# Kernel tuning notes

Hardware: AMD Instinct MI355X
Metric: run time of the kernel (lower is better)

Reference implementation:

```python
import jax, jax.numpy as jnp
import numpy as np

D_MODEL = 2048
N_HEADS = 32
N_KV_HEADS = 8
HEAD_DIM = D_MODEL // N_HEADS
ROPE_BASE = 10000.0

def setup_inputs() -> dict:
    key = jax.random.key(0)
    ks = jax.random.split(key, 5)
    B, S = 1, 2048
    x = jax.random.normal(ks[0], (B, S, D_MODEL), dtype=jnp.float32)
    sc = 1.0 / np.sqrt(D_MODEL)
    Wq = jax.random.normal(ks[1], (D_MODEL, D_MODEL), dtype=jnp.float32) * sc
    Wk = jax.random.normal(ks[2], (N_KV_HEADS * HEAD_DIM, D_MODEL), dtype=jnp.float32) * sc
    Wv = jax.random.normal(ks[3], (N_KV_HEADS * HEAD_DIM, D_MODEL), dtype=jnp.float32) * sc
    Wo = jax.random.normal(ks[4], (D_MODEL, D_MODEL), dtype=jnp.float32) * sc
    return {"x": x, "Wq": Wq, "Wk": Wk, "Wv": Wv, "Wo": Wo}

def _rope_cos_sin(seq_len, dtype):
    inv_freq = 1.0 / (ROPE_BASE ** (jnp.arange(0, HEAD_DIM, 2, dtype=jnp.float32) / HEAD_DIM))
    t = jnp.arange(seq_len, dtype=jnp.float32)
    freqs = jnp.einsum('i,j->ij', t, inv_freq)          # [S, hd/2]
    emb = jnp.concatenate([freqs, freqs], axis=-1)      # [S, hd]
    return jnp.cos(emb).astype(dtype), jnp.sin(emb).astype(dtype)

def _rotate_half(x):
    x1, x2 = x[..., : HEAD_DIM // 2], x[..., HEAD_DIM // 2 :]
    return jnp.concatenate([-x2, x1], axis=-1)

def reference(x, Wq, Wk, Wv, Wo):
    B, S, _ = x.shape
    scale = HEAD_DIM ** -0.5
    # projections (Linear: x @ W.T)
    q = (x @ Wq.T).reshape(B, S, N_HEADS, HEAD_DIM).transpose(0, 2, 1, 3)      # [B,H,S,hd]
    k = (x @ Wk.T).reshape(B, S, N_KV_HEADS, HEAD_DIM).transpose(0, 2, 1, 3)   # [B,Hkv,S,hd]
    v = (x @ Wv.T).reshape(B, S, N_KV_HEADS, HEAD_DIM).transpose(0, 2, 1, 3)
    cos, sin = _rope_cos_sin(S, x.dtype)                # [S,hd], broadcasts over B,H
    q = q * cos + _rotate_half(q) * sin
    k = k * cos + _rotate_half(k) * sin
    rep = N_HEADS // N_KV_HEADS
    k = jnp.repeat(k, rep, axis=1)                       # [B,H,S,hd]
    v = jnp.repeat(v, rep, axis=1)
    scores = jnp.einsum('bhqd,bhkd->bhqk', q, k) * scale # [B,H,S,S]
    attn = jax.nn.softmax(scores, axis=-1)
    out = jnp.einsum('bhqk,bhkd->bhqd', attn, v)         # [B,H,S,hd]
    out = out.transpose(0, 2, 1, 3).reshape(B, S, D_MODEL)
    return out @ Wo.T
```

## Files before the change

### kernel.cpp

```cpp
#include <hip/hip_runtime.h>
#include <hip/hip_bf16.h>
#include <cmath>

typedef __bf16 bf16_t;
typedef __attribute__((ext_vector_type(8))) __bf16 bf16x8;
typedef __attribute__((ext_vector_type(4))) float f32x4;
typedef __attribute__((ext_vector_type(4))) short s16x4;

#define S_LEN 2048
#define DMODEL 2048
#define KVDIM 512
#define NHEADS 32
#define NKV 8
#define HDIM 64

__device__ inline f32x4 zero4() { f32x4 z; z[0]=0.f; z[1]=0.f; z[2]=0.f; z[3]=0.f; return z; }

__global__ void convert_all(const float* __restrict__ s0, bf16_t* __restrict__ d0,
                            const float* __restrict__ s1, bf16_t* __restrict__ d1,
                            const float* __restrict__ s2, bf16_t* __restrict__ d2,
                            const float* __restrict__ s3, bf16_t* __restrict__ d3,
                            const float* __restrict__ s4, bf16_t* __restrict__ d4) {
  int b = blockIdx.x;
  const float* src; bf16_t* dst; int boff;
  if      (b < 2048) { src = s0; dst = d0; boff = b; }
  else if (b < 4096) { src = s1; dst = d1; boff = b - 2048; }
  else if (b < 4608) { src = s2; dst = d2; boff = b - 4096; }
  else if (b < 5120) { src = s3; dst = d3; boff = b - 4608; }
  else               { src = s4; dst = d4; boff = b - 5120; }
  int idx = (boff * 256 + threadIdx.x) * 8;
  bf16x8 v;
#pragma unroll
  for (int j = 0; j < 8; j++) v[j] = (bf16_t)src[idx + j];
  *(bf16x8*)(dst + idx) = v;
}

template <int BN, bool F32OUT>
__device__ __forceinline__ void gemm_core(const bf16_t* __restrict__ A,
                                          const bf16_t* __restrict__ Bt,
                                          void* __restrict__ Cout,
                                          int N, int K, int bm, int bn) {
  constexpr int NT_W = BN / 32;
  __shared__ __attribute__((aligned(16))) bf16_t As[2][128 * 64];
  __shared__ __attribute__((aligned(16))) bf16_t Bs[2][BN * 64];
  const int tid  = threadIdx.x;
  const int wave = tid >> 6, lane = tid & 63;
  const int wm = wave >> 1, wn = wave & 1;
  const int quad = lane >> 4, lr = lane & 15;
  const int srow = lane >> 3, scol = lane & 7;

  f32x4 acc[4][NT_W];
#pragma unroll
  for (int i = 0; i < 4; i++)
#pragma unroll
    for (int j = 0; j < NT_W; j++) acc[i][j] = zero4();

#define G_STAGE(BUF, K0)                                                                 \
  {                                                                                      \
    _Pragma("unroll")                                                                    \
    for (int i = 0; i < 4; i++) {                                                        \
      const bf16_t* gA = A + (size_t)(bm + i * 32 + wave * 8 + srow) * K + (K0) + scol * 8; \
      bf16_t* lA = As[BUF] + (i * 32 + wave * 8) * 64;                                   \
      __builtin_amdgcn_global_load_lds((const __attribute__((address_space(1))) void*)gA,\
                                       (__attribute__((address_space(3))) void*)lA, 16, 0, 0); \
    }                                                                                    \
    _Pragma("unroll")                                                                    \
    for (int i = 0; i < BN / 32; i++) {                                                  \
      const bf16_t* gB = Bt + (size_t)(bn + i * 32 + wave * 8 + srow) * K + (K0) + scol * 8; \
      bf16_t* lB = Bs[BUF] + (i * 32 + wave * 8) * 64;                                   \
      __builtin_amdgcn_global_load_lds((const __attribute__((address_space(1))) void*)gB,\
                                       (__attribute__((address_space(3))) void*)lB, 16, 0, 0); \
    }                                                                                    \
  }

  G_STAGE(0, 0);
  __syncthreads();

  int cur = 0;
  for (int k0 = 0; k0 < K; k0 += 64) {
    if (k0 + 64 < K) G_STAGE(cur ^ 1, k0 + 64);
#pragma unroll
    for (int ks = 0; ks < 2; ks++) {
      bf16x8 a[4], b[NT_W];
#pragma unroll
      for (int mt = 0; mt < 4; mt++)
        a[mt] = *(const bf16x8*)&As[cur][(wm * 64 + mt * 16 + lr) * 64 + ks * 32 + quad * 8];
#pragma unroll
      for (int nt = 0; nt < NT_W; nt++)
        b[nt] = *(const bf16x8*)&Bs[cur][(wn * (BN / 2) + nt * 16 + lr) * 64 + ks * 32 + quad * 8];
#pragma unroll
      for (int mt = 0; mt < 4; mt++)
#pragma unroll
        for (int nt = 0; nt < NT_W; nt++)
          acc[mt][nt] = __builtin_amdgcn_mfma_f32_16x16x32_bf16(a[mt], b[nt], acc[mt][nt], 0, 0, 0);
    }
    __syncthreads();
    cur ^= 1;
  }
#undef G_STAGE

#pragma unroll
  for (int mt = 0; mt < 4; mt++)
#pragma unroll
    for (int nt = 0; nt < NT_W; nt++)
#pragma unroll
      for (int r = 0; r < 4; r++) {
        int row = bm + wm * 64 + mt * 16 + quad * 4 + r;
        int col = bn + wn * (BN / 2) + nt * 16 + lr;
        if (F32OUT) ((float*)Cout)[(size_t)row * N + col] = acc[mt][nt][r];
        else ((bf16_t*)Cout)[(size_t)row * N + col] = (bf16_t)acc[mt][nt][r];
      }
}

__device__ __forceinline__ void xcd_tile(int b, int& bm, int& bn) {
  int c = b & 7, t = b >> 3;
  bm = (((c >> 2) << 3) + (t >> 3)) * 128;
  bn = (((c & 3) << 3) + (t & 7)) * 64;
}

__global__ __launch_bounds__(256) void gemm_proj(const bf16_t* __restrict__ xb,
                                                 const bf16_t* __restrict__ Wqb,
                                                 const bf16_t* __restrict__ Wkb,
                                                 const bf16_t* __restrict__ Wvb,
                                                 bf16_t* __restrict__ qb,
                                                 bf16_t* __restrict__ kb,
                                                 bf16_t* __restrict__ vb) {
  int b = blockIdx.x;
  if (b < 512) {
    int bm, bn;
    xcd_tile(b, bm, bn);
    gemm_core<64, false>(xb, Wqb, qb, 2048, 2048, bm, bn);
  } else if (b < 640) {
    int r = b - 512;
    gemm_core<64, false>(xb, Wkb, kb, 512, 2048, (r >> 3) * 128, (r & 7) * 64);
  } else {
    int r = b - 640;
    gemm_core<64, false>(Wvb, xb, vb, 2048, 2048, (r >> 5) * 128, (r & 31) * 64);
  }
}

__global__ __launch_bounds__(256) void gemm_out(const bf16_t* __restrict__ A,
                                                const bf16_t* __restrict__ Bt,
                                                float* __restrict__ C) {
  int bm, bn;
  xcd_tile(blockIdx.x, bm, bn);
  gemm_core<64, true>(A, Bt, C, 2048, 2048, bm, bn);
}

__global__ void rope_k(bf16_t* __restrict__ kb) {
  int idx = blockIdx.x * 256 + threadIdx.x;
  int s = idx >> 8;
  int rem = idx & 255;
  int head = rem >> 5;
  int i = rem & 31;
  float freq = __expf(-0.2878231366f * (float)i);
  float ang = (float)s * freq;
  float sn, cs;
  sincosf(ang, &sn, &cs);
  size_t base = (size_t)s * KVDIM + head * 64 + i;
  float x0 = (float)kb[base];
  float x1 = (float)kb[base + 32];
  kb[base]      = (bf16_t)(x0 * cs - x1 * sn);
  kb[base + 32] = (bf16_t)(x1 * cs + x0 * sn);
}

__global__ __launch_bounds__(256) void attn_kernel(const bf16_t* __restrict__ q,
                                                   const bf16_t* __restrict__ k,
                                                   const bf16_t* __restrict__ vT,
                                                   bf16_t* __restrict__ out) {
  __shared__ __attribute__((aligned(16))) bf16_t Ks[2][128 * 64];
  __shared__ __attribute__((aligned(16))) bf16_t Vs[2][64 * 128];
  const int tid  = threadIdx.x;
  const int wave = tid >> 6, lane = tid & 63;
  const int quad = lane >> 4, lr = lane & 15;
  const int srow = lane >> 3, scol = lane & 7;
  const int vrow = lane >> 4, vcol = lane & 15;
  const int cg = scol ^ srow;
  const int qt = blockIdx.x, h = blockIdx.y;
  const int hkv = h >> 2;
  const int qrow0 = qt * 128 + wave * 32;
  const int sw = lr & 7;
  const int c0 = (quad ^ sw) * 8;
  const int c1 = ((quad + 4) ^ sw) * 8;

  bf16x8 aqA0, aqA1, aqB0, aqB1;
#pragma unroll
  for (int set = 0; set < 2; set++) {
    int row = qrow0 + set * 16 + lr;
    const bf16_t* qp = q + (size_t)row * DMODEL + h * HDIM + quad * 8;
    bf16x8 r0 = *(const bf16x8*)qp;
    bf16x8 r1 = *(const bf16x8*)(qp + 32);
    float srow_f = (float)row;
    bf16x8 a0, a1;
#pragma unroll
    for (int j = 0; j < 8; j++) {
      float freq = __expf(-0.2878231366f * (float)(quad * 8 + j));
      float sn, cs;
      sincosf(srow_f * freq, &sn, &cs);
      float x0 = (float)r0[j], x1 = (float)r1[j];
      a0[j] = (bf16_t)(x0 * cs - x1 * sn);
      a1[j] = (bf16_t)(x1 * cs + x0 * sn);
    }
    if (set == 0) { aqA0 = a0; aqA1 = a1; } else { aqB0 = a0; aqB1 = a1; }
  }

  f32x4 OA[4], OB[4];
  float lA = 0.f, lB = 0.f;
#pragma unroll
  for (int mt = 0; mt < 4; mt++) { OA[mt] = zero4(); OB[mt] = zero4(); }

#define STAGE_TILE(BUF, KT)                                                              \
  {                                                                                      \
    _Pragma("unroll")                                                                    \
    for (int j = 0; j < 4; j++) {                                                        \
      const bf16_t* gK = k + (size_t)((KT) + wave * 32 + j * 8 + srow) * KVDIM +         \
                         hkv * HDIM + cg * 8;                                            \
      bf16_t* lK = Ks[BUF] + (wave * 32 + j * 8) * 64;                                   \
      __builtin_amdgcn_global_load_lds((const __attribute__((address_space(1))) void*)gK,\
                                       (__attribute__((address_space(3))) void*)lK, 16, 0, 0); \
    }                                                                                    \
    _Pragma("unroll")                                                                    \
    for (int j = 0; j < 4; j++) {                                                        \
      int dg = wave * 16 + j * 4 + vrow;                                                 \
      int cgv = vcol ^ (dg & 7);                                                         \
      const bf16_t* gV = vT + (size_t)(hkv * HDIM + dg) * S_LEN + (KT) + cgv * 8;        \
      bf16_t* lV = Vs[BUF] + (wave * 16 + j * 4) * 128;                                  \
      __builtin_amdgcn_global_load_lds((const __attribute__((address_space(1))) void*)gV,\
                                       (__attribute__((address_space(3))) void*)lV, 16, 0, 0); \
    }                                                                                    \
  }

  STAGE_TILE(0, 0);
  __syncthreads();

  int cur = 0;
  for (int kt = 0; kt < S_LEN; kt += 128) {
    if (kt + 128 < S_LEN) STAGE_TILE(cur ^ 1, kt + 128);
    const bf16_t* Kc = Ks[cur];
    const bf16_t* Vc = Vs[cur];

    s16x4 bpA[8], bpB[8];
#pragma unroll
    for (int nt = 0; nt < 8; nt++) {
      const int rk = (nt * 16 + lr) * 64;
      bf16x8 kb0 = *(const bf16x8*)&Kc[rk + c0];
      bf16x8 kb1 = *(const bf16x8*)&Kc[rk + c1];
      f32x4 sA = zero4(), sB = zero4();
      __builtin_amdgcn_s_setprio(1);
      sA = __builtin_amdgcn_mfma_f32_16x16x32_bf16(kb0, aqA0, sA, 0, 0, 0);
      sA = __builtin_amdgcn_mfma_f32_16x16x32_bf16(kb1, aqA1, sA, 0, 0, 0);
      sB = __builtin_amdgcn_mfma_f32_16x16x32_bf16(kb0, aqB0, sB, 0, 0, 0);
      sB = __builtin_amdgcn_mfma_f32_16x16x32_bf16(kb1, aqB1, sB, 0, 0, 0);
      __builtin_amdgcn_s_setprio(0);
#pragma unroll
      for (int r = 0; r < 4; r++) {
        float pA = __builtin_amdgcn_exp2f(sA[r] * 0.1803368801f);
        lA += pA;
        bpA[nt][r] = __builtin_bit_cast(short, (bf16_t)pA);
        float pB = __builtin_amdgcn_exp2f(sB[r] * 0.1803368801f);
        lB += pB;
        bpB[nt][r] = __builtin_bit_cast(short, (bf16_t)pB);
      }
    }
#pragma unroll
    for (int nt = 0; nt < 8; nt++) {
      const int slot = ((nt * 2 + (quad >> 1)) ^ sw) * 8 + (quad & 1) * 4;
      s16x4 av[4];
#pragma unroll
      for (int mt = 0; mt < 4; mt++)
        av[mt] = *(const s16x4*)&Vc[(mt * 16 + lr) * 128 + slot];
      __builtin_amdgcn_s_setprio(1);
#pragma unroll
      for (int mt = 0; mt < 4; mt++) {
        OA[mt] = __builtin_amdgcn_mfma_f32_16x16x16bf16_1k(av[mt], bpA[nt], OA[mt], 0, 0, 0);
        OB[mt] = __builtin_amdgcn_mfma_f32_16x16x16bf16_1k(av[mt], bpB[nt], OB[mt], 0, 0, 0);
      }
      __builtin_amdgcn_s_setprio(0);
    }
    __syncthreads();
    cur ^= 1;
  }
#undef STAGE_TILE

  lA += __shfl_xor(lA, 16);
  lA += __shfl_xor(lA, 32);
  lB += __shfl_xor(lB, 16);
  lB += __shfl_xor(lB, 32);
  float invA = 1.f / lA;
  float invB = 1.f / lB;

#pragma unroll
  for (int mt = 0; mt < 4; mt++) {
    s16x4 ovA, ovB;
#pragma unroll
    for (int r = 0; r < 4; r++) {
      ovA[r] = __builtin_bit_cast(short, (bf16_t)(OA[mt][r] * invA));
      ovB[r] = __builtin_bit_cast(short, (bf16_t)(OB[mt][r] * invB));
    }
    *(s16x4*)&out[(size_t)(qrow0 + lr) * DMODEL + h * HDIM + mt * 16 + quad * 4] = ovA;
    *(s16x4*)&out[(size_t)(qrow0 + 16 + lr) * DMODEL + h * HDIM + mt * 16 + quad * 4] = ovB;
  }
}

extern "C" void kernel_launch(void* const* d_in, const int* in_sizes, int n_in,
                              void* d_out, int out_size, void* d_ws, size_t ws_size,
                              hipStream_t stream) {
  (void)in_sizes; (void)n_in; (void)out_size; (void)ws_size;
  const float* x  = (const float*)d_in[0];
  const float* Wq = (const float*)d_in[1];
  const float* Wk = (const float*)d_in[2];
  const float* Wv = (const float*)d_in[3];
  const float* Wo = (const float*)d_in[4];

  bf16_t* xb  = (bf16_t*)d_ws;
  bf16_t* Wqb = xb  + (size_t)4 * 1024 * 1024;
  bf16_t* Wkb = Wqb + (size_t)4 * 1024 * 1024;
  bf16_t* Wvb = Wkb + (size_t)1024 * 1024;
  bf16_t* qb  = Wvb + (size_t)1024 * 1024;
  bf16_t* kb  = qb  + (size_t)4 * 1024 * 1024;
  bf16_t* vb  = kb  + (size_t)1024 * 1024;
  bf16_t* Wob = vb  + (size_t)1024 * 1024;
  bf16_t* ab  = xb;

  dim3 blk(256);
  convert_all<<<7168, blk, 0, stream>>>(x, xb, Wq, Wqb, Wk, Wkb, Wv, Wvb, Wo, Wob);
  gemm_proj<<<768, blk, 0, stream>>>(xb, Wqb, Wkb, Wvb, qb, kb, vb);
  rope_k<<<2048, blk, 0, stream>>>(kb);
  attn_kernel<<<dim3(S_LEN / 128, NHEADS), blk, 0, stream>>>(qb, kb, vb, ab);
  gemm_out<<<512, blk, 0, stream>>>(ab, Wob, (float*)d_out);
}
```

Before: 236.7 us.

## Triple-buffer GEMM LDS staging with explicit vmcnt waits and single barrier

Result: slower. 289.1 us (+22.1%).

```diff
diff --git a/kernel.cpp b/kernel.cpp
--- a/kernel.cpp
+++ b/kernel.cpp
@@ -41,8 +41,8 @@
                                           void* __restrict__ Cout,
                                           int N, int K, int bm, int bn) {
   constexpr int NT_W = BN / 32;
-  __shared__ __attribute__((aligned(16))) bf16_t As[2][128 * 64];
-  __shared__ __attribute__((aligned(16))) bf16_t Bs[2][BN * 64];
+  __shared__ __attribute__((aligned(16))) bf16_t As[3][128 * 64];
+  __shared__ __attribute__((aligned(16))) bf16_t Bs[3][BN * 64];
   const int tid  = threadIdx.x;
   const int wave = tid >> 6, lane = tid & 63;
   const int wm = wave >> 1, wn = wave & 1;
@@ -73,42 +73,51 @@
     }                                                                                    \
   }
 
+  const int nt = K / 64;
   G_STAGE(0, 0);
-  __syncthreads();
-
-  int cur = 0;
-  for (int k0 = 0; k0 < K; k0 += 64) {
-    if (k0 + 64 < K) G_STAGE(cur ^ 1, k0 + 64);
+  G_STAGE(1, 64);
+  asm volatile("s_waitcnt vmcnt(6)" ::: "memory");
+  __builtin_amdgcn_sched_barrier(0);
+  __builtin_amdgcn_s_barrier();
+
+  for (int t = 0; t < nt; ++t) {
+    if (t + 2 < nt) G_STAGE((t + 2) % 3, (t + 2) * 64);
+    const bf16_t* Ac = As[t % 3];
+    const bf16_t* Bc = Bs[t % 3];
 #pragma unroll
     for (int ks = 0; ks < 2; ks++) {
       bf16x8 a[4], b[NT_W];
 #pragma unroll
       for (int mt = 0; mt < 4; mt++)
-        a[mt] = *(const bf16x8*)&As[cur][(wm * 64 + mt * 16 + lr) * 64 + ks * 32 + quad * 8];
-#pragma unroll
-      for (int nt = 0; nt < NT_W; nt++)
-        b[nt] = *(const bf16x8*)&Bs[cur][(wn * (BN / 2) + nt * 16 + lr) * 64 + ks * 32 + quad * 8];
+        a[mt] = *(const bf16x8*)&Ac[(wm * 64 + mt * 16 + lr) * 64 + ks * 32 + quad * 8];
+#pragma unroll
+      for (int nt2 = 0; nt2 < NT_W; nt2++)
+        b[nt2] = *(const bf16x8*)&Bc[(wn * (BN / 2) + nt2 * 16 + lr) * 64 + ks * 32 + quad * 8];
 #pragma unroll
       for (int mt = 0; mt < 4; mt++)
 #pragma unroll
-        for (int nt = 0; nt < NT_W; nt++)
-          acc[mt][nt] = __builtin_amdgcn_mfma_f32_16x16x32_bf16(a[mt], b[nt], acc[mt][nt], 0, 0, 0);
-    }
-    __syncthreads();
-    cur ^= 1;
+        for (int nt2 = 0; nt2 < NT_W; nt2++)
+          acc[mt][nt2] = __builtin_amdgcn_mfma_f32_16x16x32_bf16(a[mt], b[nt2], acc[mt][nt2], 0, 0, 0);
+    }
+    if (t + 1 < nt) {
+      if (t + 2 < nt) asm volatile("s_waitcnt vmcnt(6)" ::: "memory");
+      else            asm volatile("s_waitcnt vmcnt(0)" ::: "memory");
+      __builtin_amdgcn_sched_barrier(0);
+      __builtin_amdgcn_s_barrier();
+    }
   }
 #undef G_STAGE
 
 #pragma unroll
   for (int mt = 0; mt < 4; mt++)
 #pragma unroll
-    for (int nt = 0; nt < NT_W; nt++)
+    for (int nt2 = 0; nt2 < NT_W; nt2++)
 #pragma unroll
       for (int r = 0; r < 4; r++) {
         int row = bm + wm * 64 + mt * 16 + quad * 4 + r;
-        int col = bn + wn * (BN / 2) + nt * 16 + lr;
-        if (F32OUT) ((float*)Cout)[(size_t)row * N + col] = acc[mt][nt][r];
-        else ((bf16_t*)Cout)[(size_t)row * N + col] = (bf16_t)acc[mt][nt][r];
+        int col = bn + wn * (BN / 2) + nt2 * 16 + lr;
+        if (F32OUT) ((float*)Cout)[(size_t)row * N + col] = acc[mt][nt2][r];
+        else ((bf16_t*)Cout)[(size_t)row * N + col] = (bf16_t)acc[mt][nt2][r];
       }
 }
 
```
